# Performance work log

Hardware: AMD Instinct MI355X
Metric: run time of the kernel (lower is better)

The kernel has to match this reference:

```python
import jax, jax.numpy as jnp
import numpy as np

N_NODES = 50000
N_EDGES = 800000
NODE_DIM = 128
EDGE_DIM = 64
HIDDEN = 128
OUT_DIM = 64


def graph_conv(x, W, b, src, dst, num_segments):
    # h = linear(x); out[dst] += h[src]  (scatter-add / segment-sum aggregation)
    h = x @ W + b
    return jax.ops.segment_sum(h[src], dst, num_segments=num_segments)


def setup_inputs() -> dict:
    key = jax.random.key(0)
    ks = jax.random.split(key, 12)
    s = 1.0 / np.sqrt(HIDDEN)
    return {
        "node_features": jax.random.normal(ks[0], (N_NODES, NODE_DIM), dtype=jnp.float32),
        "edge_index": jax.random.randint(ks[1], (2, N_EDGES), 0, N_NODES, dtype=jnp.int64),
        "edge_features": jax.random.normal(ks[2], (N_EDGES, EDGE_DIM), dtype=jnp.float32),
        "edge_meta_index": jax.random.randint(ks[3], (2, N_EDGES), 0, N_EDGES, dtype=jnp.int64),
        "W1": jax.random.normal(ks[4], (NODE_DIM, HIDDEN), dtype=jnp.float32) * s,
        "b1": jnp.zeros((HIDDEN,), dtype=jnp.float32),
        "W2": jax.random.normal(ks[5], (HIDDEN, HIDDEN), dtype=jnp.float32) * s,
        "b2": jnp.zeros((HIDDEN,), dtype=jnp.float32),
        "We": jax.random.normal(ks[6], (EDGE_DIM, HIDDEN), dtype=jnp.float32) * s,
        "be": jnp.zeros((HIDDEN,), dtype=jnp.float32),
        "Wfc": jax.random.normal(ks[7], (2 * HIDDEN, OUT_DIM), dtype=jnp.float32) * s,
        "bfc": jnp.zeros((OUT_DIM,), dtype=jnp.float32),
    }


def reference(node_features, edge_index, edge_features, edge_meta_index,
              W1, b1, W2, b2, We, be, Wfc, bfc):
    row, col = edge_index[0], edge_index[1]
    mrow, mcol = edge_meta_index[0], edge_meta_index[1]

    # two node GraphConvs (dropout is identity in eval / p=0)
    x = jax.nn.relu(graph_conv(node_features, W1, b1, row, col, N_NODES))
    x = jax.nn.relu(graph_conv(x, W2, b2, row, col, N_NODES))

    # edge GraphConv on the line graph: e has one row per original edge
    e = graph_conv(edge_features, We, be, mrow, mcol, N_EDGES)

    # per-edge scatter-add aggregation (vectorized form of the Python loop):
    # aggregated_neighbors[dest] += x[src]; aggregated_edges[dest] += e[idx]
    agg_neighbors = jax.ops.segment_sum(x[row], col, num_segments=N_NODES)
    agg_edges = jax.ops.segment_sum(e, col, num_segments=N_NODES)

    out = jnp.concatenate([x + agg_neighbors, agg_edges], axis=1) @ Wfc + bfc
    return out
```

## Files before the change

kernel.cpp:

```cpp
#include <hip/hip_runtime.h>

#define N_NODES 50000
#define N_EDGES 800000
#define NODE_DIM 128
#define EDGE_DIM 64
#define HIDDEN 128
#define OUT_DIM 64

#define NBKT 196
#define CAP 4864
#define EPB 4096
#define NBLK1 196

typedef unsigned short u16;
typedef unsigned int u32;

__device__ __forceinline__ float bflo(u32 u) { return __builtin_bit_cast(float, u << 16); }
__device__ __forceinline__ float bfhi(u32 u) { return __builtin_bit_cast(float, u & 0xFFFF0000u); }
__device__ __forceinline__ u32 pack2(float x, float y) {
    u32 a = __builtin_bit_cast(u32, x);
    a += 0x7FFFu + ((a >> 16) & 1u);
    u32 b = __builtin_bit_cast(u32, y);
    b += 0x7FFFu + ((b >> 16) & 1u);
    return (a >> 16) | (b & 0xFFFF0000u);
}

__global__ void init_cursors(int* __restrict__ bcur, int* __restrict__ bcurm)
{
    int t = threadIdx.x;
    if (t < NBKT) { bcur[t] = t * CAP; bcurm[t] = t * CAP; }
}

__global__ __launch_bounds__(256) void bin_pairs(
    const int* __restrict__ row, const int* __restrict__ col,
    const int* __restrict__ mrow, const int* __restrict__ mcol,
    int* __restrict__ bcur, int* __restrict__ bcurm,
    uint2* __restrict__ pairs, uint2* __restrict__ pairsm)
{
    int prob = (blockIdx.x >= NBLK1) ? 1 : 0;
    int blk = blockIdx.x - prob * NBLK1;
    int base = blk * EPB;
    int t = threadIdx.x;
    __shared__ int lh[NBKT];
    __shared__ int lbase[NBKT];
    __shared__ int lcur[NBKT];
    for (int i = t; i < NBKT; i += 256) { lh[i] = 0; lcur[i] = 0; }
    __syncthreads();
    int k[16], v[16];
    #pragma unroll
    for (int i = 0; i < 16; i++) {
        int idx = base + i * 256 + t;
        if (idx < N_EDGES) {
            if (!prob) { k[i] = col[idx]; v[i] = row[idx]; }
            else       { k[i] = col[mcol[idx]]; v[i] = mrow[idx]; }
            atomicAdd(&lh[k[i] >> 8], 1);
        } else {
            k[i] = -1; v[i] = 0;
        }
    }
    __syncthreads();
    int* gcur = prob ? bcurm : bcur;
    for (int i = t; i < NBKT; i += 256)
        lbase[i] = atomicAdd(&gcur[i], lh[i]);
    __syncthreads();
    uint2* PR = prob ? pairsm : pairs;
    #pragma unroll
    for (int i = 0; i < 16; i++) {
        if (k[i] >= 0) {
            int bk = k[i] >> 8;
            int p = lbase[bk] + atomicAdd(&lcur[bk], 1);
            if (p < (bk + 1) * CAP)
                PR[p] = make_uint2((u32)v[i], (u32)k[i]);
        }
    }
}

__global__ __launch_bounds__(256) void bucket_fill(
    const uint2* __restrict__ pairs, const uint2* __restrict__ pairsm,
    const int* __restrict__ bcur, const int* __restrict__ bcurm,
    int* __restrict__ offp, int* __restrict__ deg, int* __restrict__ ids,
    int* __restrict__ offpm, int* __restrict__ degm, int* __restrict__ idsm)
{
    int prob = (blockIdx.x >= NBKT) ? 1 : 0;
    int b = blockIdx.x - prob * NBKT;
    const uint2* PR = prob ? pairsm : pairs;
    int cnt_total = (prob ? bcurm[b] : bcur[b]) - b * CAP;
    if (cnt_total > CAP) cnt_total = CAP;
    int n0 = b << 8;
    int nn = N_NODES - n0; if (nn > 256) nn = 256;
    __shared__ int hist[256];
    __shared__ int cur[256];
    __shared__ int wsum[4];
    __shared__ uint2 pbuf[CAP];
    int t = threadIdx.x;
    hist[t] = 0;
    __syncthreads();
    for (int i = t; i < cnt_total; i += 256) {
        uint2 pr = PR[(size_t)b * CAP + i];
        pbuf[i] = pr;
        atomicAdd(&hist[(int)pr.y - n0], 1);
    }
    __syncthreads();
    int h = hist[t];
    int x = h;
    int lane = t & 63, wid = t >> 6;
    for (int d = 1; d < 64; d <<= 1) {
        int u = __shfl_up(x, d, 64);
        if (lane >= d) x += u;
    }
    if (lane == 63) wsum[wid] = x;
    __syncthreads();
    int wex = 0;
    for (int i = 0; i < wid; i++) wex += wsum[i];
    int excl = wex + x - h;
    cur[t] = excl;
    if (t < nn) {
        if (!prob) { offp[n0 + t] = b * CAP + excl; deg[n0 + t] = h; }
        else       { offpm[n0 + t] = b * CAP + excl; degm[n0 + t] = h; }
    }
    __syncthreads();
    int* OI = prob ? idsm : ids;
    for (int i = t; i < cnt_total; i += 256) {
        uint2 pr = pbuf[i];
        int p = atomicAdd(&cur[(int)pr.y - n0], 1);
        OI[(size_t)b * CAP + p] = (int)pr.x;
    }
}

__global__ __launch_bounds__(256) void precompute_wcomb(
    const float* __restrict__ We, const float* __restrict__ be,
    const float* __restrict__ Wfc, float* __restrict__ Wcomb,
    float* __restrict__ bvec)
{
    int idx = blockIdx.x * 256 + threadIdx.x;
    if (idx < 64 * 64) {
        int k = idx >> 6, c = idx & 63;
        float s = 0.f;
        for (int h = 0; h < 128; h++)
            s = fmaf(We[k * 128 + h], Wfc[(128 + h) * 64 + c], s);
        Wcomb[idx] = s;
    } else if (idx < 64 * 64 + 64) {
        int c = idx - 64 * 64;
        float s = 0.f;
        for (int h = 0; h < 128; h++)
            s = fmaf(be[h], Wfc[(128 + h) * 64 + c], s);
        bvec[c] = s;
    }
}

__global__ __launch_bounds__(256) void gemm64_f32(
    const float* __restrict__ A, const float* __restrict__ W,
    u16* __restrict__ P, int M)
{
    __shared__ float As[64][132];
    __shared__ float Ws[64][128];
    int r0 = blockIdx.x * 64;
    for (int i = threadIdx.x; i < 64 * 32; i += 256) {
        int rr = i >> 5, cc = i & 31;
        int gr = r0 + rr;
        float4 v = make_float4(0.f, 0.f, 0.f, 0.f);
        if (gr < M) v = ((const float4*)(A + (size_t)gr * 128))[cc];
        *(float4*)(&As[rr][cc * 4]) = v;
    }
    float acc[4][8];
    #pragma unroll
    for (int r = 0; r < 4; r++)
        #pragma unroll
        for (int c = 0; c < 8; c++) acc[r][c] = 0.f;
    int rg = threadIdx.x >> 4;
    int cg = threadIdx.x & 15;
    for (int kb = 0; kb < 2; kb++) {
        __syncthreads();
        for (int i = threadIdx.x; i < 64 * 32; i += 256) {
            int rr = i >> 5, cc = i & 31;
            *(float4*)(&Ws[rr][cc * 4]) =
                ((const float4*)(W + (size_t)(kb * 64 + rr) * 128))[cc];
        }
        __syncthreads();
        #pragma unroll 8
        for (int k = 0; k < 64; k++) {
            float4 w0 = *(const float4*)(&Ws[k][cg * 4]);
            float4 w1 = *(const float4*)(&Ws[k][64 + cg * 4]);
            #pragma unroll
            for (int r = 0; r < 4; r++) {
                float a = As[rg * 4 + r][kb * 64 + k];
                acc[r][0] = fmaf(a, w0.x, acc[r][0]);
                acc[r][1] = fmaf(a, w0.y, acc[r][1]);
                acc[r][2] = fmaf(a, w0.z, acc[r][2]);
                acc[r][3] = fmaf(a, w0.w, acc[r][3]);
                acc[r][4] = fmaf(a, w1.x, acc[r][4]);
                acc[r][5] = fmaf(a, w1.y, acc[r][5]);
                acc[r][6] = fmaf(a, w1.z, acc[r][6]);
                acc[r][7] = fmaf(a, w1.w, acc[r][7]);
            }
        }
    }
    #pragma unroll
    for (int r = 0; r < 4; r++) {
        int gr = r0 + rg * 4 + r;
        if (gr < M) {
            uint2 o0, o1;
            o0.x = pack2(acc[r][0], acc[r][1]);
            o0.y = pack2(acc[r][2], acc[r][3]);
            o1.x = pack2(acc[r][4], acc[r][5]);
            o1.y = pack2(acc[r][6], acc[r][7]);
            ((uint2*)(P + (size_t)gr * 128))[cg] = o0;
            ((uint2*)(P + (size_t)gr * 128 + 64))[cg] = o1;
        }
    }
}

__global__ __launch_bounds__(256) void gemm64_bf16(
    const u16* __restrict__ A, const float* __restrict__ W,
    u16* __restrict__ P, int M)
{
    __shared__ float As[64][132];
    __shared__ float Ws[64][128];
    int r0 = blockIdx.x * 64;
    for (int i = threadIdx.x; i < 64 * 32; i += 256) {
        int rr = i >> 5, cc = i & 31;
        int gr = r0 + rr;
        uint2 u = make_uint2(0u, 0u);
        if (gr < M) u = ((const uint2*)(A + (size_t)gr * 128))[cc];
        float4 v = make_float4(bflo(u.x), bfhi(u.x), bflo(u.y), bfhi(u.y));
        *(float4*)(&As[rr][cc * 4]) = v;
    }
    float acc[4][8];
    #pragma unroll
    for (int r = 0; r < 4; r++)
        #pragma unroll
        for (int c = 0; c < 8; c++) acc[r][c] = 0.f;
    int rg = threadIdx.x >> 4;
    int cg = threadIdx.x & 15;
    for (int kb = 0; kb < 2; kb++) {
        __syncthreads();
        for (int i = threadIdx.x; i < 64 * 32; i += 256) {
            int rr = i >> 5, cc = i & 31;
            *(float4*)(&Ws[rr][cc * 4]) =
                ((const float4*)(W + (size_t)(kb * 64 + rr) * 128))[cc];
        }
        __syncthreads();
        #pragma unroll 8
        for (int k = 0; k < 64; k++) {
            float4 w0 = *(const float4*)(&Ws[k][cg * 4]);
            float4 w1 = *(const float4*)(&Ws[k][64 + cg * 4]);
            #pragma unroll
            for (int r = 0; r < 4; r++) {
                float a = As[rg * 4 + r][kb * 64 + k];
                acc[r][0] = fmaf(a, w0.x, acc[r][0]);
                acc[r][1] = fmaf(a, w0.y, acc[r][1]);
                acc[r][2] = fmaf(a, w0.z, acc[r][2]);
                acc[r][3] = fmaf(a, w0.w, acc[r][3]);
                acc[r][4] = fmaf(a, w1.x, acc[r][4]);
                acc[r][5] = fmaf(a, w1.y, acc[r][5]);
                acc[r][6] = fmaf(a, w1.z, acc[r][6]);
                acc[r][7] = fmaf(a, w1.w, acc[r][7]);
            }
        }
    }
    #pragma unroll
    for (int r = 0; r < 4; r++) {
        int gr = r0 + rg * 4 + r;
        if (gr < M) {
            uint2 o0, o1;
            o0.x = pack2(acc[r][0], acc[r][1]);
            o0.y = pack2(acc[r][2], acc[r][3]);
            o1.x = pack2(acc[r][4], acc[r][5]);
            o1.y = pack2(acc[r][6], acc[r][7]);
            ((uint2*)(P + (size_t)gr * 128))[cg] = o0;
            ((uint2*)(P + (size_t)gr * 128 + 64))[cg] = o1;
        }
    }
}

__global__ __launch_bounds__(256) void agg_relu_bf16(
    const u16* __restrict__ P, const int* __restrict__ offp,
    const int* __restrict__ deg,
    const int* __restrict__ ids, const float* __restrict__ bias,
    u16* __restrict__ X, int M)
{
    int w = blockIdx.x * 4 + (threadIdx.x >> 6);
    if (w >= M) return;
    int lane = threadIdx.x & 63;
    int q = lane >> 4;
    int l = lane & 15;
    int beg = offp[w], end = beg + deg[w];
    const uint4* F = (const uint4*)P;
    float a0 = 0.f, a1 = 0.f, a2 = 0.f, a3 = 0.f,
          a4 = 0.f, a5 = 0.f, a6 = 0.f, a7 = 0.f;
    int i = beg;
    for (; i + 7 < end; i += 8) {
        int s0 = ids[i + q], s1 = ids[i + q + 4];
        uint4 v0 = F[(size_t)s0 * 16 + l];
        uint4 v1 = F[(size_t)s1 * 16 + l];
        a0 += bflo(v0.x) + bflo(v1.x); a1 += bfhi(v0.x) + bfhi(v1.x);
        a2 += bflo(v0.y) + bflo(v1.y); a3 += bfhi(v0.y) + bfhi(v1.y);
        a4 += bflo(v0.z) + bflo(v1.z); a5 += bfhi(v0.z) + bfhi(v1.z);
        a6 += bflo(v0.w) + bflo(v1.w); a7 += bfhi(v0.w) + bfhi(v1.w);
    }
    for (int j = i + q; j < end; j += 4) {
        uint4 v = F[(size_t)ids[j] * 16 + l];
        a0 += bflo(v.x); a1 += bfhi(v.x);
        a2 += bflo(v.y); a3 += bfhi(v.y);
        a4 += bflo(v.z); a5 += bfhi(v.z);
        a6 += bflo(v.w); a7 += bfhi(v.w);
    }
    a0 += __shfl_xor(a0, 32, 64); a1 += __shfl_xor(a1, 32, 64);
    a2 += __shfl_xor(a2, 32, 64); a3 += __shfl_xor(a3, 32, 64);
    a4 += __shfl_xor(a4, 32, 64); a5 += __shfl_xor(a5, 32, 64);
    a6 += __shfl_xor(a6, 32, 64); a7 += __shfl_xor(a7, 32, 64);
    a0 += __shfl_xor(a0, 16, 64); a1 += __shfl_xor(a1, 16, 64);
    a2 += __shfl_xor(a2, 16, 64); a3 += __shfl_xor(a3, 16, 64);
    a4 += __shfl_xor(a4, 16, 64); a5 += __shfl_xor(a5, 16, 64);
    a6 += __shfl_xor(a6, 16, 64); a7 += __shfl_xor(a7, 16, 64);
    if (q == 0) {
        float dg = (float)(end - beg);
        float4 b0 = ((const float4*)bias)[2 * l];
        float4 b1 = ((const float4*)bias)[2 * l + 1];
        a0 = fmaxf(fmaf(dg, b0.x, a0), 0.f);
        a1 = fmaxf(fmaf(dg, b0.y, a1), 0.f);
        a2 = fmaxf(fmaf(dg, b0.z, a2), 0.f);
        a3 = fmaxf(fmaf(dg, b0.w, a3), 0.f);
        a4 = fmaxf(fmaf(dg, b1.x, a4), 0.f);
        a5 = fmaxf(fmaf(dg, b1.y, a5), 0.f);
        a6 = fmaxf(fmaf(dg, b1.z, a6), 0.f);
        a7 = fmaxf(fmaf(dg, b1.w, a7), 0.f);
        uint4 o;
        o.x = pack2(a0, a1); o.y = pack2(a2, a3);
        o.z = pack2(a4, a5); o.w = pack2(a6, a7);
        ((uint4*)(X + (size_t)w * 128))[l] = o;
    }
}

__global__ __launch_bounds__(256) void agg_epilogue(
    const u16* __restrict__ X2, const float* __restrict__ ef,
    const int* __restrict__ offp, const int* __restrict__ deg,
    const int* __restrict__ ids,
    const int* __restrict__ offpm, const int* __restrict__ degm,
    const int* __restrict__ mids,
    u16* __restrict__ S, u16* __restrict__ Gg, int M)
{
    int w = blockIdx.x * 4 + (threadIdx.x >> 6);
    if (w >= M) return;
    int lane = threadIdx.x & 63;
    int q = lane >> 4;
    int l = lane & 15;
    {
        int beg = offp[w], end = beg + deg[w];
        const uint4* F = (const uint4*)X2;
        float a0 = 0.f, a1 = 0.f, a2 = 0.f, a3 = 0.f,
              a4 = 0.f, a5 = 0.f, a6 = 0.f, a7 = 0.f;
        int i = beg;
        for (; i + 7 < end; i += 8) {
            int s0 = ids[i + q], s1 = ids[i + q + 4];
            uint4 v0 = F[(size_t)s0 * 16 + l];
            uint4 v1 = F[(size_t)s1 * 16 + l];
            a0 += bflo(v0.x) + bflo(v1.x); a1 += bfhi(v0.x) + bfhi(v1.x);
            a2 += bflo(v0.y) + bflo(v1.y); a3 += bfhi(v0.y) + bfhi(v1.y);
            a4 += bflo(v0.z) + bflo(v1.z); a5 += bfhi(v0.z) + bfhi(v1.z);
            a6 += bflo(v0.w) + bflo(v1.w); a7 += bfhi(v0.w) + bfhi(v1.w);
        }
        for (int j = i + q; j < end; j += 4) {
            uint4 v = F[(size_t)ids[j] * 16 + l];
            a0 += bflo(v.x); a1 += bfhi(v.x);
            a2 += bflo(v.y); a3 += bfhi(v.y);
            a4 += bflo(v.z); a5 += bfhi(v.z);
            a6 += bflo(v.w); a7 += bfhi(v.w);
        }
        a0 += __shfl_xor(a0, 32, 64); a1 += __shfl_xor(a1, 32, 64);
        a2 += __shfl_xor(a2, 32, 64); a3 += __shfl_xor(a3, 32, 64);
        a4 += __shfl_xor(a4, 32, 64); a5 += __shfl_xor(a5, 32, 64);
        a6 += __shfl_xor(a6, 32, 64); a7 += __shfl_xor(a7, 32, 64);
        a0 += __shfl_xor(a0, 16, 64); a1 += __shfl_xor(a1, 16, 64);
        a2 += __shfl_xor(a2, 16, 64); a3 += __shfl_xor(a3, 16, 64);
        a4 += __shfl_xor(a4, 16, 64); a5 += __shfl_xor(a5, 16, 64);
        a6 += __shfl_xor(a6, 16, 64); a7 += __shfl_xor(a7, 16, 64);
        if (q == 0) {
            uint4 own = F[(size_t)w * 16 + l];
            a0 += bflo(own.x); a1 += bfhi(own.x);
            a2 += bflo(own.y); a3 += bfhi(own.y);
            a4 += bflo(own.z); a5 += bfhi(own.z);
            a6 += bflo(own.w); a7 += bfhi(own.w);
            uint4 o;
            o.x = pack2(a0, a1); o.y = pack2(a2, a3);
            o.z = pack2(a4, a5); o.w = pack2(a6, a7);
            ((uint4*)(S + (size_t)w * 128))[l] = o;
        }
    }
    {
        int beg = offpm[w], end = beg + degm[w];
        const float4* E = (const float4*)ef;
        float g0 = 0.f, g1 = 0.f, g2 = 0.f, g3 = 0.f;
        int i = beg;
        for (; i + 7 < end; i += 8) {
            int s0 = mids[i + q], s1 = mids[i + q + 4];
            float4 v0 = E[(size_t)s0 * 16 + l];
            float4 v1 = E[(size_t)s1 * 16 + l];
            g0 += v0.x + v1.x; g1 += v0.y + v1.y;
            g2 += v0.z + v1.z; g3 += v0.w + v1.w;
        }
        for (int j = i + q; j < end; j += 4) {
            float4 v = E[(size_t)mids[j] * 16 + l];
            g0 += v.x; g1 += v.y; g2 += v.z; g3 += v.w;
        }
        g0 += __shfl_xor(g0, 32, 64); g1 += __shfl_xor(g1, 32, 64);
        g2 += __shfl_xor(g2, 32, 64); g3 += __shfl_xor(g3, 32, 64);
        g0 += __shfl_xor(g0, 16, 64); g1 += __shfl_xor(g1, 16, 64);
        g2 += __shfl_xor(g2, 16, 64); g3 += __shfl_xor(g3, 16, 64);
        if (q == 0) {
            uint2 o;
            o.x = pack2(g0, g1); o.y = pack2(g2, g3);
            ((uint2*)(Gg + (size_t)w * 64))[l] = o;
        }
    }
}

__global__ __launch_bounds__(256) void final_gemm(
    const u16* __restrict__ S, const u16* __restrict__ Gg,
    const int* __restrict__ degm, const float* __restrict__ Wfc,
    const float* __restrict__ Wcomb, const float* __restrict__ bvec,
    const float* __restrict__ bfc, float* __restrict__ out, int M)
{
    __shared__ float Ss[64][132];
    __shared__ float Gs[64][68];
    __shared__ float Ws[64][64];
    int r0 = blockIdx.x * 64;
    for (int i = threadIdx.x; i < 64 * 32; i += 256) {
        int rr = i >> 5, cc = i & 31;
        int gr = r0 + rr;
        uint2 u = make_uint2(0u, 0u);
        if (gr < M) u = ((const uint2*)(S + (size_t)gr * 128))[cc];
        float4 v = make_float4(bflo(u.x), bfhi(u.x), bflo(u.y), bfhi(u.y));
        *(float4*)(&Ss[rr][cc * 4]) = v;
    }
    for (int i = threadIdx.x; i < 64 * 16; i += 256) {
        int rr = i >> 4, cc = i & 15;
        int gr = r0 + rr;
        uint2 u = make_uint2(0u, 0u);
        if (gr < M) u = ((const uint2*)(Gg + (size_t)gr * 64))[cc];
        float4 v = make_float4(bflo(u.x), bfhi(u.x), bflo(u.y), bfhi(u.y));
        *(float4*)(&Gs[rr][cc * 4]) = v;
    }
    float acc[4][4];
    #pragma unroll
    for (int r = 0; r < 4; r++)
        #pragma unroll
        for (int c = 0; c < 4; c++) acc[r][c] = 0.f;
    int rg = threadIdx.x >> 4;
    int cg = threadIdx.x & 15;
    for (int ph = 0; ph < 3; ph++) {
        __syncthreads();
        const float* Wsrc = (ph < 2) ? (Wfc + (size_t)ph * 64 * 64) : Wcomb;
        for (int i = threadIdx.x; i < 64 * 16; i += 256) {
            int rr = i >> 4, cc = i & 15;
            *(float4*)(&Ws[rr][cc * 4]) = ((const float4*)(Wsrc + (size_t)rr * 64))[cc];
        }
        __syncthreads();
        #pragma unroll 8
        for (int k = 0; k < 64; k++) {
            float4 wv = *(const float4*)(&Ws[k][cg * 4]);
            #pragma unroll
            for (int r = 0; r < 4; r++) {
                float a = (ph < 2) ? Ss[rg * 4 + r][ph * 64 + k] : Gs[rg * 4 + r][k];
                acc[r][0] = fmaf(a, wv.x, acc[r][0]);
                acc[r][1] = fmaf(a, wv.y, acc[r][1]);
                acc[r][2] = fmaf(a, wv.z, acc[r][2]);
                acc[r][3] = fmaf(a, wv.w, acc[r][3]);
            }
        }
    }
    float4 bv = ((const float4*)bvec)[cg];
    float4 bf = ((const float4*)bfc)[cg];
    #pragma unroll
    for (int r = 0; r < 4; r++) {
        int gr = r0 + rg * 4 + r;
        if (gr < M) {
            float cnt = (float)degm[gr];
            float4 o;
            o.x = acc[r][0] + fmaf(cnt, bv.x, bf.x);
            o.y = acc[r][1] + fmaf(cnt, bv.y, bf.y);
            o.z = acc[r][2] + fmaf(cnt, bv.z, bf.z);
            o.w = acc[r][3] + fmaf(cnt, bv.w, bf.w);
            ((float4*)(out + (size_t)gr * 64))[cg] = o;
        }
    }
}

extern "C" void kernel_launch(void* const* d_in, const int* in_sizes, int n_in,
                              void* d_out, int out_size, void* d_ws, size_t ws_size,
                              hipStream_t stream)
{
    const float* nf  = (const float*)d_in[0];
    const int*   ei  = (const int*)d_in[1];
    const float* ef  = (const float*)d_in[2];
    const int*   emi = (const int*)d_in[3];
    const float* W1  = (const float*)d_in[4];
    const float* b1  = (const float*)d_in[5];
    const float* W2  = (const float*)d_in[6];
    const float* b2  = (const float*)d_in[7];
    const float* We  = (const float*)d_in[8];
    const float* be  = (const float*)d_in[9];
    const float* Wfc = (const float*)d_in[10];
    const float* bfc = (const float*)d_in[11];

    const int* row  = ei;
    const int* col  = ei + N_EDGES;
    const int* mrow = emi;
    const int* mcol = emi + N_EDGES;

    u16* A  = (u16*)d_ws;
    u16* B  = A + (size_t)N_NODES * 128;
    u16* S  = B + (size_t)N_NODES * 128;
    u16* Gg = S + (size_t)N_NODES * 128;
    uint2* pairs  = (uint2*)(Gg + (size_t)N_NODES * 64);
    uint2* pairsm = pairs + (size_t)NBKT * CAP;
    float* Wcomb = (float*)(pairsm + (size_t)NBKT * CAP);
    float* bvec  = Wcomb + 64 * 64;
    int* offp  = (int*)(bvec + 64);
    int* deg   = offp + N_NODES;
    int* offpm = deg + N_NODES;
    int* degm  = offpm + N_NODES;
    int* bcur  = degm + N_NODES;
    int* bcurm = bcur + 256;
    int* ids   = bcurm + 256;
    int* idsm  = ids + (size_t)NBKT * CAP;

    precompute_wcomb<<<17, 256, 0, stream>>>(We, be, Wfc, Wcomb, bvec);

    init_cursors<<<1, 256, 0, stream>>>(bcur, bcurm);
    bin_pairs<<<2 * NBLK1, 256, 0, stream>>>(row, col, mrow, mcol,
                                             bcur, bcurm, pairs, pairsm);
    bucket_fill<<<2 * NBKT, 256, 0, stream>>>(pairs, pairsm, bcur, bcurm,
                                              offp, deg, ids, offpm, degm, idsm);

    gemm64_f32<<<(N_NODES + 63) / 64, 256, 0, stream>>>(nf, W1, A, N_NODES);
    agg_relu_bf16<<<(N_NODES + 3) / 4, 256, 0, stream>>>(A, offp, deg, ids, b1, B, N_NODES);
    gemm64_bf16<<<(N_NODES + 63) / 64, 256, 0, stream>>>(B, W2, A, N_NODES);
    agg_relu_bf16<<<(N_NODES + 3) / 4, 256, 0, stream>>>(A, offp, deg, ids, b2, B, N_NODES);
    agg_epilogue<<<(N_NODES + 3) / 4, 256, 0, stream>>>(
        B, ef, offp, deg, ids, offpm, degm, idsm, S, Gg, N_NODES);
    final_gemm<<<(N_NODES + 63) / 64, 256, 0, stream>>>(
        S, Gg, degm, Wfc, Wcomb, bvec, bfc, (float*)d_out, N_NODES);
}
```

Measured before the change: 562.4 us.

## Use bf16 MFMA for node and final GEMMs and pack bin pairs

Replaces the three FP32 FMA GEMMs (W1, W2, final FC) with bf16 MFMA 16x16x32 kernels. Operands are staged in XOR-swizzled shared memory, and the weights are pre-transposed and converted to bf16 in new prep kernels that also absorb cursor initialisation. The bin/bucket pairs are packed into 32 bits (source id plus local node offset) instead of uint2, halving that scratch traffic. The trade-off is lower precision: the fp32 input features and weights are now rounded to bf16. There is also an extra small prep launch.

```diff
diff --git a/kernel.cpp b/kernel.cpp
--- a/kernel.cpp
+++ b/kernel.cpp
@@ -14,6 +14,8 @@
 
 typedef unsigned short u16;
 typedef unsigned int u32;
+typedef __attribute__((ext_vector_type(8))) short bf16x8;
+typedef __attribute__((ext_vector_type(4))) float f32x4;
 
 __device__ __forceinline__ float bflo(u32 u) { return __builtin_bit_cast(float, u << 16); }
 __device__ __forceinline__ float bfhi(u32 u) { return __builtin_bit_cast(float, u & 0xFFFF0000u); }
@@ -24,18 +26,63 @@
     b += 0x7FFFu + ((b >> 16) & 1u);
     return (a >> 16) | (b & 0xFFFF0000u);
 }
-
-__global__ void init_cursors(int* __restrict__ bcur, int* __restrict__ bcurm)
-{
-    int t = threadIdx.x;
-    if (t < NBKT) { bcur[t] = t * CAP; bcurm[t] = t * CAP; }
+__device__ __forceinline__ u16 bf16r(float x) {
+    u32 a = __builtin_bit_cast(u32, x);
+    a += 0x7FFFu + ((a >> 16) & 1u);
+    return (u16)(a >> 16);
+}
+
+__global__ __launch_bounds__(256) void pre1(
+    const float* __restrict__ We, const float* __restrict__ be,
+    const float* __restrict__ Wfc, const float* __restrict__ W1,
+    const float* __restrict__ W2,
+    float* __restrict__ Wcomb, float* __restrict__ bvec,
+    short* __restrict__ W1t, short* __restrict__ W2t,
+    int* __restrict__ bcur, int* __restrict__ bcurm)
+{
+    int idx = blockIdx.x * 256 + threadIdx.x;
+    if (idx < 4096) {
+        int k = idx >> 6, c = idx & 63;
+        float s = 0.f;
+        for (int h = 0; h < 128; h++)
+            s = fmaf(We[k * 128 + h], Wfc[(128 + h) * 64 + c], s);
+        Wcomb[idx] = s;
+    } else if (idx < 4160) {
+        int c = idx - 4096;
+        float s = 0.f;
+        for (int h = 0; h < 128; h++)
+            s = fmaf(be[h], Wfc[(128 + h) * 64 + c], s);
+        bvec[c] = s;
+    } else if (idx < 20544) {
+        int i = idx - 4160; int n = i >> 7, k = i & 127;
+        W1t[n * 128 + k] = (short)bf16r(W1[k * 128 + n]);
+    } else if (idx < 36928) {
+        int i = idx - 20544; int n = i >> 7, k = i & 127;
+        W2t[n * 128 + k] = (short)bf16r(W2[k * 128 + n]);
+    } else if (idx < 37320) {
+        int i = idx - 36928;
+        if (i < 196) bcur[i] = i * CAP;
+        else bcurm[i - 196] = (i - 196) * CAP;
+    }
+}
+
+__global__ __launch_bounds__(256) void pre2(
+    const float* __restrict__ Wfc, const float* __restrict__ Wcomb,
+    short* __restrict__ Wft)
+{
+    int idx = blockIdx.x * 256 + threadIdx.x;
+    if (idx < 64 * 192) {
+        int n = idx / 192, k = idx - n * 192;
+        float v = (k < 128) ? Wfc[k * 64 + n] : Wcomb[(k - 128) * 64 + n];
+        Wft[n * 192 + k] = (short)bf16r(v);
+    }
 }
 
 __global__ __launch_bounds__(256) void bin_pairs(
     const int* __restrict__ row, const int* __restrict__ col,
     const int* __restrict__ mrow, const int* __restrict__ mcol,
     int* __restrict__ bcur, int* __restrict__ bcurm,
-    uint2* __restrict__ pairs, uint2* __restrict__ pairsm)
+    u32* __restrict__ pairs, u32* __restrict__ pairsm)
 {
     int prob = (blockIdx.x >= NBLK1) ? 1 : 0;
     int blk = blockIdx.x - prob * NBLK1;
@@ -63,27 +110,27 @@
     for (int i = t; i < NBKT; i += 256)
         lbase[i] = atomicAdd(&gcur[i], lh[i]);
     __syncthreads();
-    uint2* PR = prob ? pairsm : pairs;
+    u32* PR = prob ? pairsm : pairs;
     #pragma unroll
     for (int i = 0; i < 16; i++) {
         if (k[i] >= 0) {
             int bk = k[i] >> 8;
             int p = lbase[bk] + atomicAdd(&lcur[bk], 1);
             if (p < (bk + 1) * CAP)
-                PR[p] = make_uint2((u32)v[i], (u32)k[i]);
+                PR[p] = (u32)v[i] | ((u32)(k[i] & 255) << 24);
         }
     }
 }
 
 __global__ __launch_bounds__(256) void bucket_fill(
-    const uint2* __restrict__ pairs, const uint2* __restrict__ pairsm,
+    const u32* __restrict__ pairs, const u32* __restrict__ pairsm,
     const int* __restrict__ bcur, const int* __restrict__ bcurm,
     int* __restrict__ offp, int* __restrict__ deg, int* __restrict__ ids,
     int* __restrict__ offpm, int* __restrict__ degm, int* __restrict__ idsm)
 {
     int prob = (blockIdx.x >= NBKT) ? 1 : 0;
     int b = blockIdx.x - prob * NBKT;
-    const uint2* PR = prob ? pairsm : pairs;
+    const u32* PR = prob ? pairsm : pairs;
     int cnt_total = (prob ? bcurm[b] : bcur[b]) - b * CAP;
     if (cnt_total > CAP) cnt_total = CAP;
     int n0 = b << 8;
@@ -91,14 +138,14 @@
     __shared__ int hist[256];
     __shared__ int cur[256];
     __shared__ int wsum[4];
-    __shared__ uint2 pbuf[CAP];
+    __shared__ u32 pbuf[CAP];
     int t = threadIdx.x;
     hist[t] = 0;
     __syncthreads();
     for (int i = t; i < cnt_total; i += 256) {
-        uint2 pr = PR[(size_t)b * CAP + i];
+        u32 pr = PR[(size_t)b * CAP + i];
         pbuf[i] = pr;
-        atomicAdd(&hist[(int)pr.y - n0], 1);
+        atomicAdd(&hist[pr >> 24], 1);
     }
     __syncthreads();
     int h = hist[t];
@@ -121,156 +168,127 @@
     __syncthreads();
     int* OI = prob ? idsm : ids;
     for (int i = t; i < cnt_total; i += 256) {
-        uint2 pr = pbuf[i];
-        int p = atomicAdd(&cur[(int)pr.y - n0], 1);
-        OI[(size_t)b * CAP + p] = (int)pr.x;
-    }
-}
-
-__global__ __launch_bounds__(256) void precompute_wcomb(
-    const float* __restrict__ We, const float* __restrict__ be,
-    const float* __restrict__ Wfc, float* __restrict__ Wcomb,
-    float* __restrict__ bvec)
-{
-    int idx = blockIdx.x * 256 + threadIdx.x;
-    if (idx < 64 * 64) {
-        int k = idx >> 6, c = idx & 63;
-        float s = 0.f;
-        for (int h = 0; h < 128; h++)
-            s = fmaf(We[k * 128 + h], Wfc[(128 + h) * 64 + c], s);
-        Wcomb[idx] = s;
-    } else if (idx < 64 * 64 + 64) {
-        int c = idx - 64 * 64;
-        float s = 0.f;
-        for (int h = 0; h < 128; h++)
-            s = fmaf(be[h], Wfc[(128 + h) * 64 + c], s);
-        bvec[c] = s;
-    }
-}
-
-__global__ __launch_bounds__(256) void gemm64_f32(
-    const float* __restrict__ A, const float* __restrict__ W,
+        u32 pr = pbuf[i];
+        int p = atomicAdd(&cur[pr >> 24], 1);
+        OI[(size_t)b * CAP + p] = (int)(pr & 0xFFFFFFu);
+    }
+}
+
+__global__ __launch_bounds__(256) void gemm_mfma_f32(
+    const float* __restrict__ A, const short* __restrict__ Wt,
     u16* __restrict__ P, int M)
 {
-    __shared__ float As[64][132];
-    __shared__ float Ws[64][128];
+    __shared__ short As[64 * 128];
+    __shared__ short Ws[128 * 128];
+    int t = threadIdx.x;
     int r0 = blockIdx.x * 64;
-    for (int i = threadIdx.x; i < 64 * 32; i += 256) {
-        int rr = i >> 5, cc = i & 31;
-        int gr = r0 + rr;
+    for (int i = t; i < 64 * 32; i += 256) {
+        int row = i >> 5, c4 = i & 31;
+        int gr = r0 + row;
         float4 v = make_float4(0.f, 0.f, 0.f, 0.f);
-        if (gr < M) v = ((const float4*)(A + (size_t)gr * 128))[cc];
-        *(float4*)(&As[rr][cc * 4]) = v;
-    }
-    float acc[4][8];
-    #pragma unroll
-    for (int r = 0; r < 4; r++)
-        #pragma unroll
-        for (int c = 0; c < 8; c++) acc[r][c] = 0.f;
-    int rg = threadIdx.x >> 4;
-    int cg = threadIdx.x & 15;
-    for (int kb = 0; kb < 2; kb++) {
-        __syncthreads();
-        for (int i = threadIdx.x; i < 64 * 32; i += 256) {
-            int rr = i >> 5, cc = i & 31;
-            *(float4*)(&Ws[rr][cc * 4]) =
-                ((const float4*)(W + (size_t)(kb * 64 + rr) * 128))[cc];
-        }
-        __syncthreads();
-        #pragma unroll 8
-        for (int k = 0; k < 64; k++) {
-            float4 w0 = *(const float4*)(&Ws[k][cg * 4]);
-            float4 w1 = *(const float4*)(&Ws[k][64 + cg * 4]);
-            #pragma unroll
-            for (int r = 0; r < 4; r++) {
-                float a = As[rg * 4 + r][kb * 64 + k];
-                acc[r][0] = fmaf(a, w0.x, acc[r][0]);
-                acc[r][1] = fmaf(a, w0.y, acc[r][1]);
-                acc[r][2] = fmaf(a, w0.z, acc[r][2]);
-                acc[r][3] = fmaf(a, w0.w, acc[r][3]);
-                acc[r][4] = fmaf(a, w1.x, acc[r][4]);
-                acc[r][5] = fmaf(a, w1.y, acc[r][5]);
-                acc[r][6] = fmaf(a, w1.z, acc[r][6]);
-                acc[r][7] = fmaf(a, w1.w, acc[r][7]);
+        if (gr < M) v = ((const float4*)(A + (size_t)gr * 128))[c4];
+        uint2 u; u.x = pack2(v.x, v.y); u.y = pack2(v.z, v.w);
+        *(uint2*)((char*)As + row * 256 + ((c4 * 8) ^ ((row & 7) << 4))) = u;
+    }
+    for (int i = t; i < 128 * 16; i += 256) {
+        int row = i >> 4, c16 = i & 15;
+        uint4 u = *(const uint4*)((const char*)Wt + row * 256 + c16 * 16);
+        *(uint4*)((char*)Ws + row * 256 + ((c16 * 16) ^ ((row & 7) << 4))) = u;
+    }
+    __syncthreads();
+    int w = t >> 6, l = t & 63, lr = l & 15, q = l >> 4;
+    int rh = (w & 1) * 32, ch = (w >> 1) * 64;
+    f32x4 acc[2][4];
+    #pragma unroll
+    for (int rt = 0; rt < 2; rt++)
+        #pragma unroll
+        for (int ct = 0; ct < 4; ct++) acc[rt][ct] = (f32x4){0.f, 0.f, 0.f, 0.f};
+    #pragma unroll
+    for (int kk = 0; kk < 4; kk++) {
+        int bo = kk * 64 + q * 16;
+        bf16x8 a[2];
+        #pragma unroll
+        for (int rt = 0; rt < 2; rt++) {
+            int ar = rh + rt * 16 + lr;
+            a[rt] = *(const bf16x8*)((const char*)As + ar * 256 + (bo ^ ((ar & 7) << 4)));
+        }
+        #pragma unroll
+        for (int ct = 0; ct < 4; ct++) {
+            int br = ch + ct * 16 + lr;
+            bf16x8 b = *(const bf16x8*)((const char*)Ws + br * 256 + (bo ^ ((br & 7) << 4)));
+            acc[0][ct] = __builtin_amdgcn_mfma_f32_16x16x32_bf16(a[0], b, acc[0][ct], 0, 0, 0);
+            acc[1][ct] = __builtin_amdgcn_mfma_f32_16x16x32_bf16(a[1], b, acc[1][ct], 0, 0, 0);
+        }
+    }
+    #pragma unroll
+    for (int rt = 0; rt < 2; rt++)
+        #pragma unroll
+        for (int reg = 0; reg < 4; reg++) {
+            int gr = r0 + rh + rt * 16 + q * 4 + reg;
+            if (gr < M) {
+                #pragma unroll
+                for (int ct = 0; ct < 4; ct++)
+                    P[(size_t)gr * 128 + ch + ct * 16 + lr] = bf16r(acc[rt][ct][reg]);
             }
         }
-    }
-    #pragma unroll
-    for (int r = 0; r < 4; r++) {
-        int gr = r0 + rg * 4 + r;
-        if (gr < M) {
-            uint2 o0, o1;
-            o0.x = pack2(acc[r][0], acc[r][1]);
-            o0.y = pack2(acc[r][2], acc[r][3]);
-            o1.x = pack2(acc[r][4], acc[r][5]);
-            o1.y = pack2(acc[r][6], acc[r][7]);
-            ((uint2*)(P + (size_t)gr * 128))[cg] = o0;
-            ((uint2*)(P + (size_t)gr * 128 + 64))[cg] = o1;
-        }
-    }
-}
-
-__global__ __launch_bounds__(256) void gemm64_bf16(
-    const u16* __restrict__ A, const float* __restrict__ W,
+}
+
+__global__ __launch_bounds__(256) void gemm_mfma_bf16(
+    const u16* __restrict__ A, const short* __restrict__ Wt,
     u16* __restrict__ P, int M)
 {
-    __shared__ float As[64][132];
-    __shared__ float Ws[64][128];
+    __shared__ short As[64 * 128];
+    __shared__ short Ws[128 * 128];
+    int t = threadIdx.x;
     int r0 = blockIdx.x * 64;
-    for (int i = threadIdx.x; i < 64 * 32; i += 256) {
-        int rr = i >> 5, cc = i & 31;
-        int gr = r0 + rr;
-        uint2 u = make_uint2(0u, 0u);
-        if (gr < M) u = ((const uint2*)(A + (size_t)gr * 128))[cc];
-        float4 v = make_float4(bflo(u.x), bfhi(u.x), bflo(u.y), bfhi(u.y));
-        *(float4*)(&As[rr][cc * 4]) = v;
-    }
-    float acc[4][8];
-    #pragma unroll
-    for (int r = 0; r < 4; r++)
-        #pragma unroll
-        for (int c = 0; c < 8; c++) acc[r][c] = 0.f;
-    int rg = threadIdx.x >> 4;
-    int cg = threadIdx.x & 15;
-    for (int kb = 0; kb < 2; kb++) {
-        __syncthreads();
-        for (int i = threadIdx.x; i < 64 * 32; i += 256) {
-            int rr = i >> 5, cc = i & 31;
-            *(float4*)(&Ws[rr][cc * 4]) =
-                ((const float4*)(W + (size_t)(kb * 64 + rr) * 128))[cc];
-        }
-        __syncthreads();
-        #pragma unroll 8
-        for (int k = 0; k < 64; k++) {
-            float4 w0 = *(const float4*)(&Ws[k][cg * 4]);
-            float4 w1 = *(const float4*)(&Ws[k][64 + cg * 4]);
-            #pragma unroll
-            for (int r = 0; r < 4; r++) {
-                float a = As[rg * 4 + r][kb * 64 + k];
-                acc[r][0] = fmaf(a, w0.x, acc[r][0]);
-                acc[r][1] = fmaf(a, w0.y, acc[r][1]);
-                acc[r][2] = fmaf(a, w0.z, acc[r][2]);
-                acc[r][3] = fmaf(a, w0.w, acc[r][3]);
-                acc[r][4] = fmaf(a, w1.x, acc[r][4]);
-                acc[r][5] = fmaf(a, w1.y, acc[r][5]);
-                acc[r][6] = fmaf(a, w1.z, acc[r][6]);
-                acc[r][7] = fmaf(a, w1.w, acc[r][7]);
+    for (int i = t; i < 64 * 16; i += 256) {
+        int row = i >> 4, c16 = i & 15;
+        int gr = r0 + row;
+        uint4 u = make_uint4(0u, 0u, 0u, 0u);
+        if (gr < M) u = *(const uint4*)((const char*)A + (size_t)gr * 256 + c16 * 16);
+        *(uint4*)((char*)As + row * 256 + ((c16 * 16) ^ ((row & 7) << 4))) = u;
+    }
+    for (int i = t; i < 128 * 16; i += 256) {
+        int row = i >> 4, c16 = i & 15;
+        uint4 u = *(const uint4*)((const char*)Wt + row * 256 + c16 * 16);
+        *(uint4*)((char*)Ws + row * 256 + ((c16 * 16) ^ ((row & 7) << 4))) = u;
+    }
+    __syncthreads();
+    int w = t >> 6, l = t & 63, lr = l & 15, q = l >> 4;
+    int rh = (w & 1) * 32, ch = (w >> 1) * 64;
+    f32x4 acc[2][4];
+    #pragma unroll
+    for (int rt = 0; rt < 2; rt++)
+        #pragma unroll
+        for (int ct = 0; ct < 4; ct++) acc[rt][ct] = (f32x4){0.f, 0.f, 0.f, 0.f};
+    #pragma unroll
+    for (int kk = 0; kk < 4; kk++) {
+        int bo = kk * 64 + q * 16;
+        bf16x8 a[2];
+        #pragma unroll
+        for (int rt = 0; rt < 2; rt++) {
+            int ar = rh + rt * 16 + lr;
+            a[rt] = *(const bf16x8*)((const char*)As + ar * 256 + (bo ^ ((ar & 7) << 4)));
+        }
+        #pragma unroll
+        for (int ct = 0; ct < 4; ct++) {
+            int br = ch + ct * 16 + lr;
+            bf16x8 b = *(const bf16x8*)((const char*)Ws + br * 256 + (bo ^ ((br & 7) << 4)));
+            acc[0][ct] = __builtin_amdgcn_mfma_f32_16x16x32_bf16(a[0], b, acc[0][ct], 0, 0, 0);
+            acc[1][ct] = __builtin_amdgcn_mfma_f32_16x16x32_bf16(a[1], b, acc[1][ct], 0, 0, 0);
+        }
+    }
+    #pragma unroll
+    for (int rt = 0; rt < 2; rt++)
+        #pragma unroll
+        for (int reg = 0; reg < 4; reg++) {
+            int gr = r0 + rh + rt * 16 + q * 4 + reg;
+            if (gr < M) {
+                #pragma unroll
+                for (int ct = 0; ct < 4; ct++)
+                    P[(size_t)gr * 128 + ch + ct * 16 + lr] = bf16r(acc[rt][ct][reg]);
             }
         }
-    }
-    #pragma unroll
-    for (int r = 0; r < 4; r++) {
-        int gr = r0 + rg * 4 + r;
-        if (gr < M) {
-            uint2 o0, o1;
-            o0.x = pack2(acc[r][0], acc[r][1]);
-            o0.y = pack2(acc[r][2], acc[r][3]);
-            o1.x = pack2(acc[r][4], acc[r][5]);
-            o1.y = pack2(acc[r][6], acc[r][7]);
-            ((uint2*)(P + (size_t)gr * 128))[cg] = o0;
-            ((uint2*)(P + (size_t)gr * 128 + 64))[cg] = o1;
-        }
-    }
 }
 
 __global__ __launch_bounds__(256) void agg_relu_bf16(
@@ -415,75 +433,73 @@
     }
 }
 
-__global__ __launch_bounds__(256) void final_gemm(
+__global__ __launch_bounds__(256) void final_mfma(
     const u16* __restrict__ S, const u16* __restrict__ Gg,
-    const int* __restrict__ degm, const float* __restrict__ Wfc,
-    const float* __restrict__ Wcomb, const float* __restrict__ bvec,
-    const float* __restrict__ bfc, float* __restrict__ out, int M)
-{
-    __shared__ float Ss[64][132];
-    __shared__ float Gs[64][68];
-    __shared__ float Ws[64][64];
+    const int* __restrict__ degm, const short* __restrict__ Wft,
+    const float* __restrict__ bvec, const float* __restrict__ bfc,
+    float* __restrict__ out, int M)
+{
+    __shared__ short As[64 * 192];
+    __shared__ short Ws[64 * 192];
+    int t = threadIdx.x;
     int r0 = blockIdx.x * 64;
-    for (int i = threadIdx.x; i < 64 * 32; i += 256) {
-        int rr = i >> 5, cc = i & 31;
-        int gr = r0 + rr;
-        uint2 u = make_uint2(0u, 0u);
-        if (gr < M) u = ((const uint2*)(S + (size_t)gr * 128))[cc];
-        float4 v = make_float4(bflo(u.x), bfhi(u.x), bflo(u.y), bfhi(u.y));
-        *(float4*)(&Ss[rr][cc * 4]) = v;
-    }
-    for (int i = threadIdx.x; i < 64 * 16; i += 256) {
-        int rr = i >> 4, cc = i & 15;
-        int gr = r0 + rr;
-        uint2 u = make_uint2(0u, 0u);
-        if (gr < M) u = ((const uint2*)(Gg + (size_t)gr * 64))[cc];
-        float4 v = make_float4(bflo(u.x), bfhi(u.x), bflo(u.y), bfhi(u.y));
-        *(float4*)(&Gs[rr][cc * 4]) = v;
-    }
-    float acc[4][4];
-    #pragma unroll
-    for (int r = 0; r < 4; r++)
-        #pragma unroll
-        for (int c = 0; c < 4; c++) acc[r][c] = 0.f;
-    int rg = threadIdx.x >> 4;
-    int cg = threadIdx.x & 15;
-    for (int ph = 0; ph < 3; ph++) {
-        __syncthreads();
-        const float* Wsrc = (ph < 2) ? (Wfc + (size_t)ph * 64 * 64) : Wcomb;
-        for (int i = threadIdx.x; i < 64 * 16; i += 256) {
-            int rr = i >> 4, cc = i & 15;
-            *(float4*)(&Ws[rr][cc * 4]) = ((const float4*)(Wsrc + (size_t)rr * 64))[cc];
-        }
-        __syncthreads();
-        #pragma unroll 8
-        for (int k = 0; k < 64; k++) {
-            float4 wv = *(const float4*)(&Ws[k][cg * 4]);
-            #pragma unroll
-            for (int r = 0; r < 4; r++) {
-                float a = (ph < 2) ? Ss[rg * 4 + r][ph * 64 + k] : Gs[rg * 4 + r][k];
-                acc[r][0] = fmaf(a, wv.x, acc[r][0]);
-                acc[r][1] = fmaf(a, wv.y, acc[r][1]);
-                acc[r][2] = fmaf(a, wv.z, acc[r][2]);
-                acc[r][3] = fmaf(a, wv.w, acc[r][3]);
+    for (int i = t; i < 64 * 16; i += 256) {
+        int row = i >> 4, c16 = i & 15;
+        int gr = r0 + row;
+        uint4 u = make_uint4(0u, 0u, 0u, 0u);
+        if (gr < M) u = *(const uint4*)((const char*)S + (size_t)gr * 256 + c16 * 16);
+        *(uint4*)((char*)As + row * 384 + ((c16 * 16) ^ ((row & 7) << 4))) = u;
+    }
+    for (int i = t; i < 64 * 8; i += 256) {
+        int row = i >> 3, c16 = i & 7;
+        int gr = r0 + row;
+        uint4 u = make_uint4(0u, 0u, 0u, 0u);
+        if (gr < M) u = *(const uint4*)((const char*)Gg + (size_t)gr * 128 + c16 * 16);
+        *(uint4*)((char*)As + row * 384 + ((256 + c16 * 16) ^ ((row & 7) << 4))) = u;
+    }
+    for (int i = t; i < 64 * 24; i += 256) {
+        int row = i / 24, c16 = i - row * 24;
+        uint4 u = *(const uint4*)((const char*)Wft + row * 384 + c16 * 16);
+        *(uint4*)((char*)Ws + row * 384 + ((c16 * 16) ^ ((row & 7) << 4))) = u;
+    }
+    __syncthreads();
+    int w = t >> 6, l = t & 63, lr = l & 15, q = l >> 4;
+    int rh = (w & 1) * 32, ch = (w >> 1) * 32;
+    f32x4 acc[2][2];
+    #pragma unroll
+    for (int rt = 0; rt < 2; rt++)
+        #pragma unroll
+        for (int ct = 0; ct < 2; ct++) acc[rt][ct] = (f32x4){0.f, 0.f, 0.f, 0.f};
+    #pragma unroll
+    for (int kk = 0; kk < 6; kk++) {
+        int bo = kk * 64 + q * 16;
+        bf16x8 a[2];
+        #pragma unroll
+        for (int rt = 0; rt < 2; rt++) {
+            int ar = rh + rt * 16 + lr;
+            a[rt] = *(const bf16x8*)((const char*)As + ar * 384 + (bo ^ ((ar & 7) << 4)));
+        }
+        #pragma unroll
+        for (int ct = 0; ct < 2; ct++) {
+            int br = ch + ct * 16 + lr;
+            bf16x8 b = *(const bf16x8*)((const char*)Ws + br * 384 + (bo ^ ((br & 7) << 4)));
+            acc[0][ct] = __builtin_amdgcn_mfma_f32_16x16x32_bf16(a[0], b, acc[0][ct], 0, 0, 0);
+            acc[1][ct] = __builtin_amdgcn_mfma_f32_16x16x32_bf16(a[1], b, acc[1][ct], 0, 0, 0);
+        }
+    }
+    float bv0 = bvec[ch + lr], bv1 = bvec[ch + 16 + lr];
+    float bf0 = bfc[ch + lr],  bf1 = bfc[ch + 16 + lr];
+    #pragma unroll
+    for (int rt = 0; rt < 2; rt++)
+        #pragma unroll
+        for (int reg = 0; reg < 4; reg++) {
+            int gr = r0 + rh + rt * 16 + q * 4 + reg;
+            if (gr < M) {
+                float cnt = (float)degm[gr];
+                out[(size_t)gr * 64 + ch + lr]      = acc[rt][0][reg] + fmaf(cnt, bv0, bf0);
+                out[(size_t)gr * 64 + ch + 16 + lr] = acc[rt][1][reg] + fmaf(cnt, bv1, bf1);
             }
         }
-    }
-    float4 bv = ((const float4*)bvec)[cg];
-    float4 bf = ((const float4*)bfc)[cg];
-    #pragma unroll
-    for (int r = 0; r < 4; r++) {
-        int gr = r0 + rg * 4 + r;
-        if (gr < M) {
-            float cnt = (float)degm[gr];
-            float4 o;
-            o.x = acc[r][0] + fmaf(cnt, bv.x, bf.x);
-            o.y = acc[r][1] + fmaf(cnt, bv.y, bf.y);
-            o.z = acc[r][2] + fmaf(cnt, bv.z, bf.z);
-            o.w = acc[r][3] + fmaf(cnt, bv.w, bf.w);
-            ((float4*)(out + (size_t)gr * 64))[cg] = o;
-        }
-    }
 }
 
 extern "C" void kernel_launch(void* const* d_in, const int* in_sizes, int n_in,
@@ -512,11 +528,14 @@
     u16* B  = A + (size_t)N_NODES * 128;
     u16* S  = B + (size_t)N_NODES * 128;
     u16* Gg = S + (size_t)N_NODES * 128;
-    uint2* pairs  = (uint2*)(Gg + (size_t)N_NODES * 64);
-    uint2* pairsm = pairs + (size_t)NBKT * CAP;
+    u32* pairs  = (u32*)(Gg + (size_t)N_NODES * 64);
+    u32* pairsm = pairs + (size_t)NBKT * CAP;
     float* Wcomb = (float*)(pairsm + (size_t)NBKT * CAP);
     float* bvec  = Wcomb + 64 * 64;
-    int* offp  = (int*)(bvec + 64);
+    short* W1t = (short*)(bvec + 64);
+    short* W2t = W1t + 128 * 128;
+    short* Wft = W2t + 128 * 128;
+    int* offp  = (int*)(Wft + 64 * 192);
     int* deg   = offp + N_NODES;
     int* offpm = deg + N_NODES;
     int* degm  = offpm + N_NODES;
@@ -525,20 +544,20 @@
     int* ids   = bcurm + 256;
     int* idsm  = ids + (size_t)NBKT * CAP;
 
-    precompute_wcomb<<<17, 256, 0, stream>>>(We, be, Wfc, Wcomb, bvec);
-
-    init_cursors<<<1, 256, 0, stream>>>(bcur, bcurm);
+    pre1<<<146, 256, 0, stream>>>(We, be, Wfc, W1, W2, Wcomb, bvec, W1t, W2t, bcur, bcurm);
+
     bin_pairs<<<2 * NBLK1, 256, 0, stream>>>(row, col, mrow, mcol,
                                              bcur, bcurm, pairs, pairsm);
     bucket_fill<<<2 * NBKT, 256, 0, stream>>>(pairs, pairsm, bcur, bcurm,
                                               offp, deg, ids, offpm, degm, idsm);
-
-    gemm64_f32<<<(N_NODES + 63) / 64, 256, 0, stream>>>(nf, W1, A, N_NODES);
+    pre2<<<48, 256, 0, stream>>>(Wfc, Wcomb, Wft);
+
+    gemm_mfma_f32<<<(N_NODES + 63) / 64, 256, 0, stream>>>(nf, W1t, A, N_NODES);
     agg_relu_bf16<<<(N_NODES + 3) / 4, 256, 0, stream>>>(A, offp, deg, ids, b1, B, N_NODES);
-    gemm64_bf16<<<(N_NODES + 63) / 64, 256, 0, stream>>>(B, W2, A, N_NODES);
+    gemm_mfma_bf16<<<(N_NODES + 63) / 64, 256, 0, stream>>>(B, W2t, A, N_NODES);
     agg_relu_bf16<<<(N_NODES + 3) / 4, 256, 0, stream>>>(A, offp, deg, ids, b2, B, N_NODES);
     agg_epilogue<<<(N_NODES + 3) / 4, 256, 0, stream>>>(
         B, ef, offp, deg, ids, offpm, degm, idsm, S, Gg, N_NODES);
-    final_gemm<<<(N_NODES + 63) / 64, 256, 0, stream>>>(
-        S, Gg, degm, Wfc, Wcomb, bvec, bfc, (float*)d_out, N_NODES);
-}
+    final_mfma<<<(N_NODES + 63) / 64, 256, 0, stream>>>(
+        S, Gg, degm, Wft, bvec, bfc, (float*)d_out, N_NODES);
+}
```

New measurement: 493.1 us. 12.3% less time.
